# Optimization experiments

Hardware: AMD Instinct MI355X
Metric: run time of the kernel (lower is better)

Reference implementation:

```python
import jax, jax.numpy as jnp
import numpy as np

B, C, L = 16, 256, 2048

def setup_inputs() -> dict:
    key = jax.random.key(0)
    y = jax.random.normal(key, (B, C, L), dtype=jnp.float32)
    alpha = jnp.float32(0.5)
    beta = jnp.float32(0.5)
    gamma = jnp.float32(0.0)
    return {"y": y, "alpha": alpha, "beta": beta, "gamma": gamma}

def reference(y, alpha, beta, gamma):
    # y: [B, C, L]
    Bs, Cs, Ls = y.shape
    # channel attention: scores over channels, scaled by 1/sqrt(L)
    scale_c = 1.0 / np.sqrt(max(Ls, 1)).astype(np.float32)
    scores_c = jnp.einsum('bcl,bdl->bcd', y, y) * scale_c          # [B, C, C]
    attn_c = jax.nn.softmax(scores_c, axis=-1)
    y_c = jnp.einsum('bcd,bdl->bcl', attn_c, y)                    # [B, C, L]
    # time attention: scores over time steps, scaled by 1/sqrt(C)
    scale_t = 1.0 / np.sqrt(max(Cs, 1)).astype(np.float32)
    scores_t = jnp.einsum('bcl,bcm->blm', y, y) * scale_t          # [B, L, L]
    attn_t = jax.nn.softmax(scores_t, axis=-1)
    y_t = jnp.einsum('blm,bcm->bcl', attn_t, y)                    # [B, C, L]
    # learnable weighted combine + residual (gamma)
    out = alpha * y_c + beta * y_t + gamma * y
    return out
```

## Files before the change

kernel.cpp:

```cpp
#include <hip/hip_runtime.h>

#define B_ 16
#define C_ 256
#define L_ 2048

typedef __attribute__((ext_vector_type(8))) short short8;
typedef __attribute__((ext_vector_type(4))) float float4v;

__device__ inline float4v mfma16(short8 a, short8 b, float4v c) {
  return __builtin_amdgcn_mfma_f32_16x16x32_bf16(a, b, c, 0, 0, 0);
}

__device__ inline ushort f2bf(float x) {
  union { float f; unsigned u; } v; v.f = x;
  unsigned r = (v.u + 0x7fffu + ((v.u >> 16) & 1u)) >> 16;
  return (ushort)r;
}

__device__ inline float bf2f(ushort u) {
  union { unsigned u; float f; } v; v.u = ((unsigned)u) << 16;
  return v.f;
}

__device__ inline void dma16(const ushort* g, void* l) {
  __builtin_amdgcn_global_load_lds(
      (const __attribute__((address_space(1))) unsigned int*)(g),
      (__attribute__((address_space(3))) unsigned int*)(l), 16, 0, 0);
}

#define BAR_FULL() asm volatile("s_waitcnt vmcnt(0) lgkmcnt(0)\ns_barrier" ::: "memory")
#define BAR_LGKM() asm volatile("s_waitcnt lgkmcnt(0)\ns_barrier" ::: "memory")

__global__ __launch_bounds__(256) void cvt_kernel(const float* __restrict__ y,
                                                  ushort* __restrict__ yb,
                                                  ushort* __restrict__ ytb) {
  __shared__ float tile[32][33];
  int b = blockIdx.z, ct = blockIdx.y, lt = blockIdx.x;
  int tx = threadIdx.x & 31, ty = threadIdx.x >> 5;
  size_t base = ((size_t)b * C_ + (size_t)ct * 32) * L_ + (size_t)lt * 32;
#pragma unroll
  for (int i = 0; i < 4; ++i) {
    int r = ty + i * 8;
    float v = y[base + (size_t)r * L_ + tx];
    tile[r][tx] = v;
    yb[base + (size_t)r * L_ + tx] = f2bf(v);
  }
  __syncthreads();
  size_t tbase = ((size_t)b * L_ + (size_t)lt * 32) * C_ + (size_t)ct * 32;
#pragma unroll
  for (int i = 0; i < 4; ++i) {
    int r = ty + i * 8;
    ytb[tbase + (size_t)r * C_ + tx] = f2bf(tile[tx][r]);
  }
}

__global__ __launch_bounds__(256) void pk_kernel(const ushort* __restrict__ yb,
                                                 ushort* __restrict__ Pc,
                                                 float* __restrict__ ginvC) {
  const int blk = blockIdx.x;
  const int b = (blk & 7) + 8 * ((blk >> 3) & 1);
  const int m0 = (blk >> 4) * 16;
  const int tid = threadIdx.x;
  const int w = tid >> 6, lane = tid & 63, quad = lane >> 4, l16 = lane & 15;
  const float scale = 0.022097086912079608f;
  const float SHIFT = 45.0f;

  __shared__ __align__(16) unsigned char Tb[2][32768];
  __shared__ float wsum[4][16];

  const ushort* Yb = yb + (size_t)b * C_ * L_;
  const int chq = ((lane & 3) - ((lane >> 3) & 3)) & 3;
  const int dl = (lane >> 2) * L_ + chq * 8;
  const int sK = (quad + ((l16 >> 1) & 3)) & 3;
  const int frag_lane = l16 * 64 + sK * 16;

  float4v acc[4];
#pragma unroll
  for (int nt = 0; nt < 4; ++nt) acc[nt] = (float4v){0.f, 0.f, 0.f, 0.f};

#pragma unroll
  for (int j = 0; j < 8; ++j) {
    int gi = w * 8 + j, kk2 = gi >> 4, chgrp = gi & 15;
    dma16(Yb + (size_t)chgrp * 16 * L_ + kk2 * 32 + dl, (void*)(Tb[0] + gi * 1024));
  }

  for (int c = 0; c < 32; ++c) {
    BAR_FULL();
    if (c < 31) {
      int kc = (c + 1) * 64;
      unsigned char* bp = Tb[(c + 1) & 1];
#pragma unroll
      for (int j = 0; j < 8; ++j) {
        int gi = w * 8 + j, kk2 = gi >> 4, chgrp = gi & 15;
        dma16(Yb + (size_t)chgrp * 16 * L_ + kc + kk2 * 32 + dl, (void*)(bp + gi * 1024));
      }
    }
    const unsigned char* cbuf = Tb[c & 1];
#pragma unroll
    for (int kk2 = 0; kk2 < 2; ++kk2) {
      short8 aA = *(const short8*)(cbuf + (kk2 * 16 + (m0 >> 4)) * 1024 + frag_lane);
#pragma unroll
      for (int nt = 0; nt < 4; ++nt) {
        short8 bB = *(const short8*)(cbuf + (kk2 * 16 + w * 4 + nt) * 1024 + frag_lane);
        acc[nt] = mfma16(aA, bB, acc[nt]);
      }
    }
  }

  float p[4][4], rs[4] = {0.f, 0.f, 0.f, 0.f};
#pragma unroll
  for (int nt = 0; nt < 4; ++nt)
#pragma unroll
    for (int r = 0; r < 4; ++r) {
      p[nt][r] = __expf(fmaf(acc[nt][r], scale, -SHIFT));
      rs[r] += p[nt][r];
    }
  ushort* Pb = Pc + ((size_t)b * 256 + m0) * 256;
#pragma unroll
  for (int nt = 0; nt < 4; ++nt)
#pragma unroll
    for (int r = 0; r < 4; ++r)
      Pb[(quad * 4 + r) * 256 + w * 64 + nt * 16 + l16] = f2bf(p[nt][r]);
#pragma unroll
  for (int r = 0; r < 4; ++r)
#pragma unroll
    for (int off = 1; off < 16; off <<= 1) rs[r] += __shfl_xor(rs[r], off);
  if (l16 == 0) {
#pragma unroll
    for (int r = 0; r < 4; ++r) wsum[w][quad * 4 + r] = rs[r];
  }
  __syncthreads();
  if (tid < 16)
    ginvC[b * 256 + m0 + tid] =
        1.0f / (wsum[0][tid] + wsum[1][tid] + wsum[2][tid] + wsum[3][tid]);
}

__global__ __launch_bounds__(256, 2) void ct_kernel(
    const ushort* __restrict__ yb, const ushort* __restrict__ ytb,
    const ushort* __restrict__ Pc, const float* __restrict__ ginvC,
    float* __restrict__ out, const float* __restrict__ alpha_p,
    const float* __restrict__ beta_p, const float* __restrict__ gamma_p) {
  const int blk = blockIdx.x;
  const int b = (blk & 7) + 8 * ((blk >> 3) & 1);
  const int m0 = (blk >> 4) * 64;
  const int tid = threadIdx.x;
  const int w = tid >> 6, lane = tid & 63, quad = lane >> 4, l16 = lane & 15;
  const int mtw = w >> 1, kt2 = w & 1;
  const float scale = 0.0625f;
  const float SHIFT = 16.0f;

  __shared__ __align__(16) unsigned char buf[2][32768];
  __shared__ ushort Pd[64 * 40];
  __shared__ float wsum[4][64];
  __shared__ float ginv[64];

  const ushort* Yt = ytb + (size_t)b * L_ * C_;
  const ushort* Yb = yb + (size_t)b * C_ * L_;
  const ushort* Pcb = Pc + (size_t)b * 256 * 256;
  const int chq = ((lane & 3) - ((lane >> 3) & 3)) & 3;
  const int klK = (lane >> 2) * C_ + chq * 8;
  const int vlV = (lane >> 2) * L_ + chq * 8;
  const int pcl = (lane >> 2) * 256 + chq * 8;
  const int sK = (quad + ((l16 >> 1) & 3)) & 3;
  const int frag_lane = l16 * 64 + sK * 16;

  short8 Qf[2][8];
#pragma unroll
  for (int mt = 0; mt < 2; ++mt)
#pragma unroll
    for (int kk = 0; kk < 8; ++kk)
      Qf[mt][kk] = *(const short8*)(Yt + (size_t)(m0 + mtw * 32 + mt * 16 + l16) * C_ +
                                    kk * 32 + quad * 8);
  const ushort* qgrow[2];
#pragma unroll
  for (int mt = 0; mt < 2; ++mt)
    qgrow[mt] = Yt + (size_t)(m0 + (1 - mtw) * 32 + mt * 16 + l16) * C_ + quad * 8;

  float4v fc[4][4];
#pragma unroll
  for (int mt = 0; mt < 4; ++mt)
#pragma unroll
    for (int nt = 0; nt < 4; ++nt) fc[mt][nt] = (float4v){0.f, 0.f, 0.f, 0.f};

  short8 qg[2][2];
#pragma unroll
  for (int mt = 0; mt < 2; ++mt) qg[0][mt] = *(const short8*)(qgrow[mt]);
#pragma unroll
  for (int j = 0; j < 4; ++j) {
    int gi = w * 4 + j;
    dma16(Pcb + (size_t)(gi * 16) * 256 + pcl, (void*)(buf[0] + gi * 1024));
  }

  for (int c2 = 0; c2 < 8; ++c2) {
    const int cb = c2 & 1;
    BAR_FULL();
    if (c2 < 7) {
      unsigned char* bp = buf[cb ^ 1];
#pragma unroll
      for (int j = 0; j < 4; ++j) {
        int gi = w * 4 + j;
        dma16(Pcb + (size_t)(gi * 16) * 256 + (c2 + 1) * 32 + pcl,
              (void*)(bp + gi * 1024));
      }
#pragma unroll
      for (int mt = 0; mt < 2; ++mt)
        qg[cb ^ 1][mt] = *(const short8*)(qgrow[mt] + (c2 + 1) * 32);
    }
#pragma unroll
    for (int mt = 0; mt < 4; ++mt) {
      short8 Ac = *(const short8*)(buf[cb] + (w * 4 + mt) * 1024 + frag_lane);
#pragma unroll
      for (int nt = 0; nt < 4; ++nt) {
        short8 Bq = ((nt >> 1) == mtw) ? Qf[nt & 1][c2] : qg[cb][nt & 1];
        fc[mt][nt] = mfma16(Ac, Bq, fc[mt][nt]);
      }
    }
  }

  const ushort* dp[8];
#pragma unroll
  for (int j = 0; j < 8; ++j) {
    int gi = w * 8 + j;
    if (gi < 16) {
      int kk = gi >> 1, g = gi & 1;
      dp[j] = Yt + (size_t)(g * 16) * C_ + kk * 32 + klK;
    } else {
      int cg = gi - 16;
      dp[j] = Yb + (size_t)cg * 16 * L_ + vlV;
    }
  }
  const int dstride = (w < 2) ? 32 * C_ : 32;

  float4v ft[4][4];
#pragma unroll
  for (int mt = 0; mt < 4; ++mt)
#pragma unroll
    for (int nt = 0; nt < 4; ++nt) ft[mt][nt] = (float4v){0.f, 0.f, 0.f, 0.f};
  float rs[2][4] = {{0.f, 0.f, 0.f, 0.f}, {0.f, 0.f, 0.f, 0.f}};

#pragma unroll
  for (int j = 0; j < 8; ++j) {
    dma16(dp[j], (void*)(buf[0] + (w * 8 + j) * 1024));
    dp[j] += dstride;
  }

  for (int c = 0; c < 64; ++c) {
    const int cb = c & 1;
    BAR_FULL();
    if (c < 63) {
      unsigned char* bp = buf[cb ^ 1];
#pragma unroll
      for (int j = 0; j < 8; ++j) {
        dma16(dp[j], (void*)(bp + (w * 8 + j) * 1024));
        dp[j] += dstride;
      }
    }
    float4v s0 = (float4v){0.f, 0.f, 0.f, 0.f};
    float4v s1 = (float4v){0.f, 0.f, 0.f, 0.f};
#pragma unroll
    for (int kk = 0; kk < 8; ++kk) {
      short8 bf = *(const short8*)(buf[cb] + (kk * 2 + kt2) * 1024 + frag_lane);
      s0 = mfma16(Qf[0][kk], bf, s0);
      s1 = mfma16(Qf[1][kk], bf, s1);
    }
#pragma unroll
    for (int mt = 0; mt < 2; ++mt) {
      float4v s = mt ? s1 : s0;
#pragma unroll
      for (int r = 0; r < 4; ++r) {
        float p = __expf(fmaf(s[r], scale, -SHIFT));
        rs[mt][r] += p;
        Pd[(mtw * 32 + mt * 16 + quad * 4 + r) * 40 + kt2 * 16 + l16] = f2bf(p);
      }
    }
    BAR_LGKM();
#pragma unroll
    for (int mt = 0; mt < 4; ++mt) {
      short8 va = *(const short8*)(buf[cb] + (16 + w * 4 + mt) * 1024 + frag_lane);
#pragma unroll
      for (int nt = 0; nt < 4; ++nt) {
        short8 pb = *(const short8*)(&Pd[(nt * 16 + l16) * 40 + quad * 8]);
        ft[mt][nt] = mfma16(va, pb, ft[mt][nt]);
      }
    }
  }

  __syncthreads();
#pragma unroll
  for (int mt = 0; mt < 2; ++mt)
#pragma unroll
    for (int r = 0; r < 4; ++r)
#pragma unroll
      for (int off = 1; off < 16; off <<= 1) rs[mt][r] += __shfl_xor(rs[mt][r], off);
  if (l16 == 0) {
#pragma unroll
    for (int mt = 0; mt < 2; ++mt)
#pragma unroll
      for (int r = 0; r < 4; ++r)
        wsum[w][mtw * 32 + mt * 16 + quad * 4 + r] = rs[mt][r];
  }
  __syncthreads();
  if (tid < 64) {
    int mh = tid >> 5;
    ginv[tid] = 1.0f / (wsum[mh * 2][tid] + wsum[mh * 2 + 1][tid]);
  }
  __syncthreads();

  const float alpha = alpha_p[0], beta = beta_p[0], gamma = gamma_p[0];
  float gq[4];
#pragma unroll
  for (int nt = 0; nt < 4; ++nt) gq[nt] = beta * ginv[nt * 16 + l16];
  float gc[4][4];
#pragma unroll
  for (int mt = 0; mt < 4; ++mt)
#pragma unroll
    for (int r = 0; r < 4; ++r)
      gc[mt][r] = alpha * ginvC[b * 256 + w * 64 + mt * 16 + quad * 4 + r];

  if (gamma != 0.0f) {
#pragma unroll
    for (int mt = 0; mt < 4; ++mt)
#pragma unroll
      for (int nt = 0; nt < 4; ++nt)
#pragma unroll
        for (int r = 0; r < 4; ++r) {
          int ch = w * 64 + mt * 16 + quad * 4 + r;
          size_t idx = ((size_t)b * C_ + ch) * L_ + m0 + nt * 16 + l16;
          float v = gc[mt][r] * fc[mt][nt][r] + gq[nt] * ft[mt][nt][r];
          out[idx] = fmaf(gamma, bf2f(Yb[(size_t)ch * L_ + m0 + nt * 16 + l16]), v);
        }
  } else {
#pragma unroll
    for (int mt = 0; mt < 4; ++mt)
#pragma unroll
      for (int nt = 0; nt < 4; ++nt)
#pragma unroll
        for (int r = 0; r < 4; ++r) {
          int ch = w * 64 + mt * 16 + quad * 4 + r;
          size_t idx = ((size_t)b * C_ + ch) * L_ + m0 + nt * 16 + l16;
          out[idx] = gc[mt][r] * fc[mt][nt][r] + gq[nt] * ft[mt][nt][r];
        }
  }
}

extern "C" void kernel_launch(void* const* d_in, const int* in_sizes, int n_in,
                              void* d_out, int out_size, void* d_ws, size_t ws_size,
                              hipStream_t stream) {
  const float* y = (const float*)d_in[0];
  const float* alpha = (const float*)d_in[1];
  const float* beta = (const float*)d_in[2];
  const float* gamma = (const float*)d_in[3];
  float* out = (float*)d_out;

  ushort* yb = (ushort*)d_ws;
  ushort* ytb = yb + (size_t)B_ * C_ * L_;
  ushort* Pc = ytb + (size_t)B_ * C_ * L_;
  float* ginvC = (float*)(Pc + (size_t)B_ * 256 * 256);

  hipLaunchKernelGGL(cvt_kernel, dim3(L_ / 32, C_ / 32, B_), dim3(256), 0, stream,
                     y, yb, ytb);
  hipLaunchKernelGGL(pk_kernel, dim3(256), dim3(256), 0, stream, yb, Pc, ginvC);
  hipLaunchKernelGGL(ct_kernel, dim3(512), dim3(256), 0, stream,
                     yb, ytb, Pc, ginvC, out, alpha, beta, gamma);
}
```

Before: 217.1 us.

## Triple-buffer DMA pipelines, 2D-tile channel scores, vectorize conversion transpose

The conversion kernel now handles 64x64 tiles with float4 loads, short8 stores and a bf16 LDS transpose. The channel-score kernel switches to 64x64 output tiles split over the K range, with atomic row-sum accumulation into a buffer zeroed by a new kernel. Both it and the main fused kernel move to a three-stage DMA ring with partial vmcnt waits, so loads stay in flight across the barrier. The main kernel drops its two-blocks-per-CU launch bound and uses 96KB+ of LDS, which may cut occupancy.

After: 291.6 us. 1.34x slower.

```diff
diff --git a/kernel.cpp b/kernel.cpp
--- a/kernel.cpp
+++ b/kernel.cpp
@@ -31,113 +31,129 @@
 #define BAR_FULL() asm volatile("s_waitcnt vmcnt(0) lgkmcnt(0)\ns_barrier" ::: "memory")
 #define BAR_LGKM() asm volatile("s_waitcnt lgkmcnt(0)\ns_barrier" ::: "memory")
 
+__global__ __launch_bounds__(256) void zk_kernel(float* __restrict__ p) {
+  p[blockIdx.x * 256 + threadIdx.x] = 0.0f;
+}
+
 __global__ __launch_bounds__(256) void cvt_kernel(const float* __restrict__ y,
                                                   ushort* __restrict__ yb,
                                                   ushort* __restrict__ ytb) {
-  __shared__ float tile[32][33];
-  int b = blockIdx.z, ct = blockIdx.y, lt = blockIdx.x;
-  int tx = threadIdx.x & 31, ty = threadIdx.x >> 5;
-  size_t base = ((size_t)b * C_ + (size_t)ct * 32) * L_ + (size_t)lt * 32;
+  __shared__ ushort tile[64][66];
+  const int b = blockIdx.z, ct = blockIdx.y, lt = blockIdx.x;
+  const int tid = threadIdx.x;
+  const int r = tid >> 2, cg = tid & 3;
+
+  size_t ybase = ((size_t)b * C_ + ct * 64 + r) * L_ + lt * 64 + cg * 16;
+  const float4* yp = (const float4*)(y + ybase);
+  ushort u[16];
 #pragma unroll
   for (int i = 0; i < 4; ++i) {
-    int r = ty + i * 8;
-    float v = y[base + (size_t)r * L_ + tx];
-    tile[r][tx] = v;
-    yb[base + (size_t)r * L_ + tx] = f2bf(v);
-  }
+    float4 v = yp[i];
+    u[i * 4 + 0] = f2bf(v.x);
+    u[i * 4 + 1] = f2bf(v.y);
+    u[i * 4 + 2] = f2bf(v.z);
+    u[i * 4 + 3] = f2bf(v.w);
+  }
+  short8 s0, s1;
+#pragma unroll
+  for (int i = 0; i < 8; ++i) { s0[i] = (short)u[i]; s1[i] = (short)u[8 + i]; }
+  *(short8*)(yb + ybase) = s0;
+  *(short8*)(yb + ybase + 8) = s1;
+#pragma unroll
+  for (int i = 0; i < 16; ++i) tile[r][cg * 16 + i] = u[i];
   __syncthreads();
-  size_t tbase = ((size_t)b * L_ + (size_t)lt * 32) * C_ + (size_t)ct * 32;
-#pragma unroll
-  for (int i = 0; i < 4; ++i) {
-    int r = ty + i * 8;
-    ytb[tbase + (size_t)r * C_ + tx] = f2bf(tile[tx][r]);
-  }
+  ushort t[16];
+#pragma unroll
+  for (int i = 0; i < 16; ++i) t[i] = tile[cg * 16 + i][r];
+  short8 t0, t1;
+#pragma unroll
+  for (int i = 0; i < 8; ++i) { t0[i] = (short)t[i]; t1[i] = (short)t[8 + i]; }
+  size_t tbase = ((size_t)b * L_ + lt * 64 + r) * C_ + ct * 64 + cg * 16;
+  *(short8*)(ytb + tbase) = t0;
+  *(short8*)(ytb + tbase + 8) = t1;
 }
 
 __global__ __launch_bounds__(256) void pk_kernel(const ushort* __restrict__ yb,
                                                  ushort* __restrict__ Pc,
-                                                 float* __restrict__ ginvC) {
+                                                 float* __restrict__ Ssum) {
   const int blk = blockIdx.x;
   const int b = (blk & 7) + 8 * ((blk >> 3) & 1);
-  const int m0 = (blk >> 4) * 16;
+  const int rest = blk >> 4;
+  const int m0 = (rest & 3) * 64, k0 = (rest >> 2) * 64;
   const int tid = threadIdx.x;
   const int w = tid >> 6, lane = tid & 63, quad = lane >> 4, l16 = lane & 15;
   const float scale = 0.022097086912079608f;
   const float SHIFT = 45.0f;
 
-  __shared__ __align__(16) unsigned char Tb[2][32768];
-  __shared__ float wsum[4][16];
+  __shared__ __align__(16) unsigned char Tb[3][16384];
 
   const ushort* Yb = yb + (size_t)b * C_ * L_;
   const int chq = ((lane & 3) - ((lane >> 3) & 3)) & 3;
-  const int dl = (lane >> 2) * L_ + chq * 8;
   const int sK = (quad + ((l16 >> 1) & 3)) & 3;
   const int frag_lane = l16 * 64 + sK * 16;
 
+  const ushort* dp[4];
+#pragma unroll
+  for (int j = 0; j < 4; ++j) {
+    int gi = w * 4 + j;
+    int base = (gi < 8) ? m0 : k0;
+    int g2 = gi & 7, rg = g2 >> 1, kk2 = g2 & 1;
+    dp[j] = Yb + (size_t)(base + rg * 16 + (lane >> 2)) * L_ + kk2 * 32 + chq * 8;
+  }
+#pragma unroll
+  for (int j = 0; j < 4; ++j) { dma16(dp[j], (void*)(Tb[0] + (w * 4 + j) * 1024)); dp[j] += 64; }
+#pragma unroll
+  for (int j = 0; j < 4; ++j) { dma16(dp[j], (void*)(Tb[1] + (w * 4 + j) * 1024)); dp[j] += 64; }
+
   float4v acc[4];
 #pragma unroll
   for (int nt = 0; nt < 4; ++nt) acc[nt] = (float4v){0.f, 0.f, 0.f, 0.f};
 
-#pragma unroll
-  for (int j = 0; j < 8; ++j) {
-    int gi = w * 8 + j, kk2 = gi >> 4, chgrp = gi & 15;
-    dma16(Yb + (size_t)chgrp * 16 * L_ + kk2 * 32 + dl, (void*)(Tb[0] + gi * 1024));
-  }
-
   for (int c = 0; c < 32; ++c) {
-    BAR_FULL();
-    if (c < 31) {
-      int kc = (c + 1) * 64;
-      unsigned char* bp = Tb[(c + 1) & 1];
-#pragma unroll
-      for (int j = 0; j < 8; ++j) {
-        int gi = w * 8 + j, kk2 = gi >> 4, chgrp = gi & 15;
-        dma16(Yb + (size_t)chgrp * 16 * L_ + kc + kk2 * 32 + dl, (void*)(bp + gi * 1024));
-      }
-    }
-    const unsigned char* cbuf = Tb[c & 1];
+    if (c < 31) { asm volatile("s_waitcnt vmcnt(4)" ::: "memory"); }
+    else        { asm volatile("s_waitcnt vmcnt(0)" ::: "memory"); }
+    asm volatile("s_barrier" ::: "memory");
+    if (c + 2 < 32) {
+      unsigned char* bp = Tb[(c + 2) % 3];
+#pragma unroll
+      for (int j = 0; j < 4; ++j) { dma16(dp[j], (void*)(bp + (w * 4 + j) * 1024)); dp[j] += 64; }
+    }
+    const unsigned char* cbuf = Tb[c % 3];
 #pragma unroll
     for (int kk2 = 0; kk2 < 2; ++kk2) {
-      short8 aA = *(const short8*)(cbuf + (kk2 * 16 + (m0 >> 4)) * 1024 + frag_lane);
+      short8 aA = *(const short8*)(cbuf + (w * 2 + kk2) * 1024 + frag_lane);
 #pragma unroll
       for (int nt = 0; nt < 4; ++nt) {
-        short8 bB = *(const short8*)(cbuf + (kk2 * 16 + w * 4 + nt) * 1024 + frag_lane);
+        short8 bB = *(const short8*)(cbuf + (8 + nt * 2 + kk2) * 1024 + frag_lane);
         acc[nt] = mfma16(aA, bB, acc[nt]);
       }
     }
   }
 
-  float p[4][4], rs[4] = {0.f, 0.f, 0.f, 0.f};
+  float rs[4] = {0.f, 0.f, 0.f, 0.f};
+  ushort* Pb = Pc + ((size_t)b * 256 + m0 + w * 16) * 256 + k0;
 #pragma unroll
   for (int nt = 0; nt < 4; ++nt)
 #pragma unroll
     for (int r = 0; r < 4; ++r) {
-      p[nt][r] = __expf(fmaf(acc[nt][r], scale, -SHIFT));
-      rs[r] += p[nt][r];
-    }
-  ushort* Pb = Pc + ((size_t)b * 256 + m0) * 256;
-#pragma unroll
-  for (int nt = 0; nt < 4; ++nt)
-#pragma unroll
-    for (int r = 0; r < 4; ++r)
-      Pb[(quad * 4 + r) * 256 + w * 64 + nt * 16 + l16] = f2bf(p[nt][r]);
+      float p = __expf(fmaf(acc[nt][r], scale, -SHIFT));
+      rs[r] += p;
+      Pb[(size_t)(quad * 4 + r) * 256 + nt * 16 + l16] = f2bf(p);
+    }
 #pragma unroll
   for (int r = 0; r < 4; ++r)
 #pragma unroll
     for (int off = 1; off < 16; off <<= 1) rs[r] += __shfl_xor(rs[r], off);
   if (l16 == 0) {
 #pragma unroll
-    for (int r = 0; r < 4; ++r) wsum[w][quad * 4 + r] = rs[r];
-  }
-  __syncthreads();
-  if (tid < 16)
-    ginvC[b * 256 + m0 + tid] =
-        1.0f / (wsum[0][tid] + wsum[1][tid] + wsum[2][tid] + wsum[3][tid]);
-}
-
-__global__ __launch_bounds__(256, 2) void ct_kernel(
+    for (int r = 0; r < 4; ++r)
+      atomicAdd(&Ssum[b * 256 + m0 + w * 16 + quad * 4 + r], rs[r]);
+  }
+}
+
+__global__ __launch_bounds__(256) void ct_kernel(
     const ushort* __restrict__ yb, const ushort* __restrict__ ytb,
-    const ushort* __restrict__ Pc, const float* __restrict__ ginvC,
+    const ushort* __restrict__ Pc, const float* __restrict__ Ssum,
     float* __restrict__ out, const float* __restrict__ alpha_p,
     const float* __restrict__ beta_p, const float* __restrict__ gamma_p) {
   const int blk = blockIdx.x;
@@ -149,7 +165,7 @@
   const float scale = 0.0625f;
   const float SHIFT = 16.0f;
 
-  __shared__ __align__(16) unsigned char buf[2][32768];
+  __shared__ __align__(16) unsigned char buf[3][32768];
   __shared__ ushort Pd[64 * 40];
   __shared__ float wsum[4][64];
   __shared__ float ginv[64];
@@ -238,28 +254,27 @@
     for (int nt = 0; nt < 4; ++nt) ft[mt][nt] = (float4v){0.f, 0.f, 0.f, 0.f};
   float rs[2][4] = {{0.f, 0.f, 0.f, 0.f}, {0.f, 0.f, 0.f, 0.f}};
 
-#pragma unroll
-  for (int j = 0; j < 8; ++j) {
-    dma16(dp[j], (void*)(buf[0] + (w * 8 + j) * 1024));
-    dp[j] += dstride;
-  }
+  BAR_LGKM();
+#pragma unroll
+  for (int j = 0; j < 8; ++j) { dma16(dp[j], (void*)(buf[0] + (w * 8 + j) * 1024)); dp[j] += dstride; }
+#pragma unroll
+  for (int j = 0; j < 8; ++j) { dma16(dp[j], (void*)(buf[1] + (w * 8 + j) * 1024)); dp[j] += dstride; }
 
   for (int c = 0; c < 64; ++c) {
-    const int cb = c & 1;
-    BAR_FULL();
-    if (c < 63) {
-      unsigned char* bp = buf[cb ^ 1];
-#pragma unroll
-      for (int j = 0; j < 8; ++j) {
-        dma16(dp[j], (void*)(bp + (w * 8 + j) * 1024));
-        dp[j] += dstride;
-      }
-    }
+    if (c < 63) { asm volatile("s_waitcnt vmcnt(8)" ::: "memory"); }
+    else        { asm volatile("s_waitcnt vmcnt(0)" ::: "memory"); }
+    asm volatile("s_barrier" ::: "memory");
+    if (c + 2 < 64) {
+      unsigned char* bp = buf[(c + 2) % 3];
+#pragma unroll
+      for (int j = 0; j < 8; ++j) { dma16(dp[j], (void*)(bp + (w * 8 + j) * 1024)); dp[j] += dstride; }
+    }
+    const unsigned char* cbuf = buf[c % 3];
     float4v s0 = (float4v){0.f, 0.f, 0.f, 0.f};
     float4v s1 = (float4v){0.f, 0.f, 0.f, 0.f};
 #pragma unroll
     for (int kk = 0; kk < 8; ++kk) {
-      short8 bf = *(const short8*)(buf[cb] + (kk * 2 + kt2) * 1024 + frag_lane);
+      short8 bf = *(const short8*)(cbuf + (kk * 2 + kt2) * 1024 + frag_lane);
       s0 = mfma16(Qf[0][kk], bf, s0);
       s1 = mfma16(Qf[1][kk], bf, s1);
     }
@@ -276,7 +291,7 @@
     BAR_LGKM();
 #pragma unroll
     for (int mt = 0; mt < 4; ++mt) {
-      short8 va = *(const short8*)(buf[cb] + (16 + w * 4 + mt) * 1024 + frag_lane);
+      short8 va = *(const short8*)(cbuf + (16 + w * 4 + mt) * 1024 + frag_lane);
 #pragma unroll
       for (int nt = 0; nt < 4; ++nt) {
         short8 pb = *(const short8*)(&Pd[(nt * 16 + l16) * 40 + quad * 8]);
@@ -315,7 +330,7 @@
   for (int mt = 0; mt < 4; ++mt)
 #pragma unroll
     for (int r = 0; r < 4; ++r)
-      gc[mt][r] = alpha * ginvC[b * 256 + w * 64 + mt * 16 + quad * 4 + r];
+      gc[mt][r] = alpha / Ssum[b * 256 + w * 64 + mt * 16 + quad * 4 + r];
 
   if (gamma != 0.0f) {
 #pragma unroll
@@ -355,11 +370,12 @@
   ushort* yb = (ushort*)d_ws;
   ushort* ytb = yb + (size_t)B_ * C_ * L_;
   ushort* Pc = ytb + (size_t)B_ * C_ * L_;
-  float* ginvC = (float*)(Pc + (size_t)B_ * 256 * 256);
-
-  hipLaunchKernelGGL(cvt_kernel, dim3(L_ / 32, C_ / 32, B_), dim3(256), 0, stream,
+  float* Ssum = (float*)(Pc + (size_t)B_ * 256 * 256);
+
+  hipLaunchKernelGGL(zk_kernel, dim3(16), dim3(256), 0, stream, Ssum);
+  hipLaunchKernelGGL(cvt_kernel, dim3(L_ / 64, C_ / 64, B_), dim3(256), 0, stream,
                      y, yb, ytb);
-  hipLaunchKernelGGL(pk_kernel, dim3(256), dim3(256), 0, stream, yb, Pc, ginvC);
+  hipLaunchKernelGGL(pk_kernel, dim3(256), dim3(256), 0, stream, yb, Pc, Ssum);
   hipLaunchKernelGGL(ct_kernel, dim3(512), dim3(256), 0, stream,
-                     yb, ytb, Pc, ginvC, out, alpha, beta, gamma);
-}
+                     yb, ytb, Pc, Ssum, out, alpha, beta, gamma);
+}
```
